# Kernel tuning notes

Hardware: AMD Instinct MI355X
Metric: run time of the kernel (lower is better)

## Reference

```python
import jax, jax.numpy as jnp
import numpy as np

D_MODEL = 256
NUM_HEADS = 8
DIM_HEAD = D_MODEL // NUM_HEADS
EPS = 1e-6
MASK_BIAS = -1.0e9


def setup_inputs() -> dict:
    key = jax.random.key(0)
    ks = jax.random.split(key, 10)
    B, S = 2, 4096
    x = jax.random.normal(ks[0], (B, S, D_MODEL), dtype=jnp.float32)
    pad_mask = jnp.zeros((B, S), dtype=jnp.float32)  # 1.0 => padded position
    scale = 1.0 / np.sqrt(D_MODEL)
    Wq = jax.random.normal(ks[1], (D_MODEL, D_MODEL), dtype=jnp.float32) * scale
    bq = jnp.zeros((D_MODEL,), dtype=jnp.float32)
    Wk = jax.random.normal(ks[2], (D_MODEL, D_MODEL), dtype=jnp.float32) * scale
    bk = jnp.zeros((D_MODEL,), dtype=jnp.float32)
    Wv = jax.random.normal(ks[3], (D_MODEL, D_MODEL), dtype=jnp.float32) * scale
    bv = jnp.zeros((D_MODEL,), dtype=jnp.float32)
    gamma = jnp.ones((D_MODEL,), dtype=jnp.float32)
    beta = jnp.zeros((D_MODEL,), dtype=jnp.float32)
    return {"x": x, "pad_mask": pad_mask, "Wq": Wq, "bq": bq, "Wk": Wk,
            "bk": bk, "Wv": Wv, "bv": bv, "gamma": gamma, "beta": beta}


def _layer_norm(h, gamma, beta):
    mu = jnp.mean(h, axis=-1, keepdims=True)
    var = jnp.mean(jnp.square(h - mu), axis=-1, keepdims=True)
    return gamma * (h - mu) * jax.lax.rsqrt(var + EPS) + beta


def reference(x, pad_mask, Wq, bq, Wk, bk, Wv, bv, gamma, beta):
    B, S, D = x.shape
    q = x @ Wq + bq  # [B,S,D]
    k = x @ Wk + bk
    v = x @ Wv + bv
    # split heads: [B,S,D] -> [B,H,S,Dh]
    def split(t):
        return t.reshape(B, S, NUM_HEADS, DIM_HEAD).transpose(0, 2, 1, 3)
    qh, kh, vh = split(q), split(k), split(v)
    w = jnp.einsum("bhqd,bhkd->bhqk", qh, kh)  # [B,H,S,S]
    # faithful to source: mask added BEFORE the 1/sqrt(dim_head) scaling
    w = w + pad_mask[:, None, None, :] * MASK_BIAS
    w = w / jnp.sqrt(jnp.float32(DIM_HEAD))
    attn = jax.nn.softmax(w, axis=-1)
    # dropout is identity at inference
    out = jnp.einsum("bhqk,bhkd->bhqd", attn, vh)  # [B,H,S,Dh]
    out = out.transpose(0, 2, 1, 3).reshape(B, S, D)
    return _layer_norm(out + x, gamma, beta)
```

## Files before the change

### kernel.cpp

```cpp
#include <hip/hip_runtime.h>
#include <hip/hip_bf16.h>

#define D_MODEL 256
#define NUM_HEADS 8
#define DIM_HEAD 32
#define SEQ 4096
#define BATCH 2
#define NROWS (BATCH * SEQ)
#define LN_EPS 1e-6f
#define MASK_BIAS -1.0e9f
#define SCALE 0.17677669529663687f
#define LOG2E 1.4426950408889634f

typedef __attribute__((ext_vector_type(8))) short short8;
typedef __attribute__((ext_vector_type(4))) float f32x4;

static __device__ __forceinline__ unsigned short f2b(float f) {
    union { __hip_bfloat16 b; unsigned short u; } cv;
    cv.b = __float2bfloat16(f);
    return cv.u;
}
static __device__ __forceinline__ unsigned int pk_bf16(float lo, float hi) {
    union { __hip_bfloat162 v; unsigned int u; } cv;
    cv.v = __float22bfloat162_rn(make_float2(lo, hi));
    return cv.u;
}
static __device__ __forceinline__ float exp2_raw(float x) {
#if __has_builtin(__builtin_amdgcn_exp2f)
    return __builtin_amdgcn_exp2f(x);
#else
    float r;
    asm volatile("v_exp_f32 %0, %1" : "=v"(r) : "v"(x));
    return r;
#endif
}
static __device__ __forceinline__ void load_lds16(const void* g, void* l) {
    __builtin_amdgcn_global_load_lds(
        (const __attribute__((address_space(1))) unsigned int*)g,
        (__attribute__((address_space(3))) unsigned int*)l, 16, 0, 0);
}

__global__ __launch_bounds__(256) void prep_kernel(
    const float* __restrict__ Wq, const float* __restrict__ Wk,
    const float* __restrict__ Wv,
    const float* __restrict__ bq, const float* __restrict__ bk,
    const float* __restrict__ bv,
    const float* __restrict__ pad,
    unsigned short* __restrict__ Wt, float* __restrict__ biasc,
    float* __restrict__ T2)
{
    const int blk = blockIdx.x;
    const int t = threadIdx.x;
    if (blk < 768) {
        const int w = blk >> 8;
        const int k = blk & 255;
        const float* W = (w == 0) ? Wq : (w == 1) ? Wk : Wv;
        Wt[(size_t)(w * 256 + t) * 256 + k] = f2b(W[(size_t)k * 256 + t]);
        if (k == 0) {
            const float* bb = (w == 0) ? bq : (w == 1) ? bk : bv;
            biasc[w * 256 + t] = bb[t];
        }
    } else {
        const int i = (blk - 768) * 256 + t;
        T2[i] = pad[i] * (MASK_BIAS * SCALE * LOG2E);
    }
}

__global__ __launch_bounds__(256) void qkv_mfma_kernel(
    const float* __restrict__ x, const unsigned short* __restrict__ Wt,
    const float* __restrict__ biasc,
    unsigned short* __restrict__ Qh, unsigned short* __restrict__ Kh,
    unsigned short* __restrict__ Vt)
{
    const int lane = threadIdx.x & 63;
    const int wid  = threadIdx.x >> 6;
    const int c    = lane & 15;
    const int quad = lane >> 4;

    const int r0 = (blockIdx.x >> 3) * 64 + wid * 16;
    const int n0 = (blockIdx.x & 7) * 96;

    f32x4 acc[6];
    float bias[6];
    #pragma unroll
    for (int t = 0; t < 6; t++) {
        acc[t] = (f32x4){0.f, 0.f, 0.f, 0.f};
        bias[t] = biasc[n0 + 16 * t + c];
    }

    const float* xp0 = x + (size_t)(r0 + c) * D_MODEL + quad * 8;
    const unsigned short* wp0 = Wt + (size_t)(n0 + c) * 256 + quad * 8;

    for (int k0 = 0; k0 < 256; k0 += 32) {
        const float4 a0 = *(const float4*)(xp0 + k0);
        const float4 a1 = *(const float4*)(xp0 + k0 + 4);
        union { unsigned int u[4]; short8 s; } af;
        af.u[0] = pk_bf16(a0.x, a0.y);
        af.u[1] = pk_bf16(a0.z, a0.w);
        af.u[2] = pk_bf16(a1.x, a1.y);
        af.u[3] = pk_bf16(a1.z, a1.w);
        #pragma unroll
        for (int t = 0; t < 6; t++) {
            const short8 bf = *(const short8*)(wp0 + (size_t)(16 * t) * 256 + k0);
            acc[t] = __builtin_amdgcn_mfma_f32_16x16x32_bf16(af.s, bf, acc[t], 0, 0, 0);
        }
    }

    #pragma unroll
    for (int t = 0; t < 6; t++) {
        const int col = n0 + 16 * t;
        const int mm  = col >> 8;
        const int dim = (col & 255) + c;
        const int h = dim >> 5, d = dim & 31;
        const int row = r0 + quad * 4;
        const int bb = row >> 12;
        const int s  = row & (SEQ - 1);
        const size_t bh = (size_t)(bb * NUM_HEADS + h);
        const float v0 = acc[t][0] + bias[t];
        const float v1 = acc[t][1] + bias[t];
        const float v2 = acc[t][2] + bias[t];
        const float v3 = acc[t][3] + bias[t];
        if (mm == 2) {
            uint2 pk = make_uint2(pk_bf16(v0, v1), pk_bf16(v2, v3));
            *(uint2*)(Vt + (bh * DIM_HEAD + d) * SEQ + s) = pk;
        } else {
            unsigned short* P = (mm == 0 ? Qh : Kh) + (bh * SEQ + s) * DIM_HEAD + d;
            P[0]  = f2b(v0);
            P[32] = f2b(v1);
            P[64] = f2b(v2);
            P[96] = f2b(v3);
        }
    }
}

__global__ __launch_bounds__(256, 4) void attn_mfma_kernel(
    const unsigned short* __restrict__ Qh, const unsigned short* __restrict__ Kh,
    const unsigned short* __restrict__ Vt, const float* __restrict__ T2,
    float* __restrict__ O)
{
    __shared__ __align__(16) unsigned short ldsK[2][64 * 32];
    __shared__ __align__(16) unsigned short ldsV[2][32 * 64];
    __shared__ __align__(16) float          ldsT[2][64];

    const int lane = threadIdx.x & 63;
    const int wid  = threadIdx.x >> 6;
    const int c    = lane & 15;
    const int quad = lane >> 4;

    const int gw = blockIdx.x;
    const int q0 = (gw & 63) * 64;
    const int h  = (gw >> 6) & (NUM_HEADS - 1);
    const int b  = gw >> 9;
    const size_t bh = (size_t)(b * NUM_HEADS + h);

    const float k2 = SCALE * LOG2E;
    const int perm = ((c & 12) << 1) | (c & 3);

    const unsigned short* Kb = Kh + bh * SEQ * DIM_HEAD;
    const unsigned short* Vb = Vt + bh * DIM_HEAD * SEQ;
    const float* Tb = T2 + (size_t)b * SEQ;

    const int qrow = q0 + wid * 16;
    const short8 qf = *(const short8*)(Qh + (bh * SEQ + qrow + c) * DIM_HEAD + quad * 8);

    union { unsigned int u[4]; short8 s; } ones;
    ones.u[0] = ones.u[1] = ones.u[2] = ones.u[3] = 0x3F803F80u;

    const int f0 = ((perm >> 1) ^ (perm >> 3)) & 3;
    const int f1 = (((perm + 4) >> 1) ^ ((perm + 4) >> 3)) & 3;
    const int kA = perm * 32 + ((quad ^ f0) << 3);
    const int kB = (perm + 4) * 32 + ((quad ^ f1) << 3);
    const int g0 = quad ^ (c & 7);
    const int vA0 = c * 64 + (g0 << 3);
    const int vA1 = c * 64 + ((g0 ^ 4) << 3);
    const int vB0 = (16 + c) * 64 + (g0 << 3);
    const int vB1 = (16 + c) * 64 + ((g0 ^ 4) << 3);

    const int skey = (lane >> 2);
    const int sgK  = lane & 3;
    const int sdim = lane >> 3;
    const int sgV  = lane & 7;

    f32x4 o0 = {0.f,0.f,0.f,0.f}, o1 = {0.f,0.f,0.f,0.f};
    f32x4 lacc = {0.f,0.f,0.f,0.f};
    const f32x4 z = {0.f, 0.f, 0.f, 0.f};

    auto stage = [&](int ch, int pb) {
        const int s0 = ch * 64;
        if (wid < 2) {
            #pragma unroll
            for (int jj = 0; jj < 2; jj++) {
                const int j = wid * 2 + jj;
                const int key = j * 16 + skey;
                const int f = ((key >> 1) ^ (key >> 3)) & 3;
                load_lds16(Kb + (size_t)(s0 + key) * 32 + ((sgK ^ f) << 3),
                           &ldsK[pb][j * 512]);
            }
        } else {
            #pragma unroll
            for (int jj = 0; jj < 2; jj++) {
                const int j = (wid - 2) * 2 + jj;
                const int dim = j * 8 + sdim;
                load_lds16(Vb + (size_t)dim * SEQ + s0 + ((sgV ^ (dim & 7)) << 3),
                           &ldsV[pb][j * 512]);
            }
            if (wid == 3 && lane < 16)
                load_lds16(Tb + s0 + lane * 4, &ldsT[pb][0]);
        }
    };

    auto sub = [&](int pb, int s) {
        const short8 kf0 = *(const short8*)&ldsK[pb][s * 1024 + kA];
        const short8 kf1 = *(const short8*)&ldsK[pb][s * 1024 + kB];
        const short8 vf0 = *(const short8*)&ldsV[pb][s ? vA1 : vA0];
        const short8 vf1 = *(const short8*)&ldsV[pb][s ? vB1 : vB0];
        const float4 t0 = *(const float4*)&ldsT[pb][s * 32 + quad * 8];
        const float4 t1 = *(const float4*)&ldsT[pb][s * 32 + quad * 8 + 4];

        const f32x4 st0 = __builtin_amdgcn_mfma_f32_16x16x32_bf16(kf0, qf, z, 0, 0, 0);
        const f32x4 st1 = __builtin_amdgcn_mfma_f32_16x16x32_bf16(kf1, qf, z, 0, 0, 0);

        float p[8];
        p[0] = exp2_raw(fmaf(st0[0], k2, t0.x));
        p[1] = exp2_raw(fmaf(st0[1], k2, t0.y));
        p[2] = exp2_raw(fmaf(st0[2], k2, t0.z));
        p[3] = exp2_raw(fmaf(st0[3], k2, t0.w));
        p[4] = exp2_raw(fmaf(st1[0], k2, t1.x));
        p[5] = exp2_raw(fmaf(st1[1], k2, t1.y));
        p[6] = exp2_raw(fmaf(st1[2], k2, t1.z));
        p[7] = exp2_raw(fmaf(st1[3], k2, t1.w));

        union { unsigned int u[4]; short8 s8; } pf;
        pf.u[0] = pk_bf16(p[0], p[1]);
        pf.u[1] = pk_bf16(p[2], p[3]);
        pf.u[2] = pk_bf16(p[4], p[5]);
        pf.u[3] = pk_bf16(p[6], p[7]);

        lacc = __builtin_amdgcn_mfma_f32_16x16x32_bf16(ones.s, pf.s8, lacc, 0, 0, 0);
        o0   = __builtin_amdgcn_mfma_f32_16x16x32_bf16(vf0,   pf.s8, o0,   0, 0, 0);
        o1   = __builtin_amdgcn_mfma_f32_16x16x32_bf16(vf1,   pf.s8, o1,   0, 0, 0);
    };

    stage(0, 0);
    __syncthreads();
    for (int ch = 0; ch < SEQ / 64; ++ch) {
        const int pb = ch & 1;
        stage((ch + 1) & 63, pb ^ 1);
        sub(pb, 0);
        sub(pb, 1);
        __syncthreads();
    }

    const float inv = 1.0f / lacc[0];
    float* op = O + ((size_t)(b * SEQ) + qrow + c) * D_MODEL + h * DIM_HEAD + quad * 4;
    *(float4*)op        = make_float4(o0[0]*inv, o0[1]*inv, o0[2]*inv, o0[3]*inv);
    *(float4*)(op + 16) = make_float4(o1[0]*inv, o1[1]*inv, o1[2]*inv, o1[3]*inv);
}

__global__ __launch_bounds__(256) void ln_kernel(
    float* AO,
    const float* __restrict__ x,
    const float* __restrict__ gamma, const float* __restrict__ beta)
{
    const int lane = threadIdx.x & 63;
    const int wid  = threadIdx.x >> 6;
    const size_t row = (size_t)blockIdx.x * 4 + wid;

    const float4 a  = ((const float4*)(AO + row * D_MODEL))[lane];
    const float4 xv = ((const float4*)(x + row * D_MODEL))[lane];
    float hv[4];
    hv[0] = a.x + xv.x;
    hv[1] = a.y + xv.y;
    hv[2] = a.z + xv.z;
    hv[3] = a.w + xv.w;

    float s = hv[0] + hv[1] + hv[2] + hv[3];
    #pragma unroll
    for (int off = 32; off > 0; off >>= 1) s += __shfl_xor(s, off, 64);
    const float mu = s * (1.0f / D_MODEL);

    float d0 = hv[0]-mu, d1 = hv[1]-mu, d2 = hv[2]-mu, d3 = hv[3]-mu;
    float ss = d0*d0 + d1*d1 + d2*d2 + d3*d3;
    #pragma unroll
    for (int off = 32; off > 0; off >>= 1) ss += __shfl_xor(ss, off, 64);
    const float rs = rsqrtf(ss * (1.0f / D_MODEL) + LN_EPS);

    const float4 g  = ((const float4*)gamma)[lane];
    const float4 bb = ((const float4*)beta)[lane];
    float4 y;
    y.x = g.x * d0 * rs + bb.x;
    y.y = g.y * d1 * rs + bb.y;
    y.z = g.z * d2 * rs + bb.z;
    y.w = g.w * d3 * rs + bb.w;
    ((float4*)(AO + row * D_MODEL))[lane] = y;
}

extern "C" void kernel_launch(void* const* d_in, const int* in_sizes, int n_in,
                              void* d_out, int out_size, void* d_ws, size_t ws_size,
                              hipStream_t stream)
{
    const float* x     = (const float*)d_in[0];
    const float* pad   = (const float*)d_in[1];
    const float* Wq    = (const float*)d_in[2];
    const float* bq    = (const float*)d_in[3];
    const float* Wk    = (const float*)d_in[4];
    const float* bk    = (const float*)d_in[5];
    const float* Wv    = (const float*)d_in[6];
    const float* bv    = (const float*)d_in[7];
    const float* gamma = (const float*)d_in[8];
    const float* beta  = (const float*)d_in[9];

    const size_t elems = (size_t)NROWS * D_MODEL;
    unsigned short* Qh = (unsigned short*)d_ws;
    unsigned short* Kh = Qh + elems;
    unsigned short* Vt = Kh + elems;
    float* T2 = (float*)(Vt + elems);
    unsigned short* Wt = (unsigned short*)(T2 + NROWS);
    float* biasc = (float*)(Wt + 768 * 256);
    float* AO = (float*)d_out;

    prep_kernel<<<800, 256, 0, stream>>>(Wq, Wk, Wv, bq, bk, bv, pad,
                                         Wt, biasc, T2);
    qkv_mfma_kernel<<<(NROWS / 64) * 8, 256, 0, stream>>>(x, Wt, biasc,
                                                          Qh, Kh, Vt);
    attn_mfma_kernel<<<BATCH * NUM_HEADS * (SEQ / 64), 256, 0, stream>>>(
        Qh, Kh, Vt, T2, AO);
    ln_kernel<<<NROWS / 4, 256, 0, stream>>>(AO, x, gamma, beta);
}
```

Measured before the change: 190.1 us.

## Triple-buffer K/V staging with explicit waitcnt and fold score scale into Q

The attention loop moves from double to triple buffering of K/V/mask tiles in LDS. It prefetches two chunks ahead and synchronises with manual s_waitcnt vmcnt plus a raw s_barrier, replacing __syncthreads. Separately, the softmax scale times log2e is folded into Q in the projection kernel, and the mask term is fed as the MFMA accumulator init, removing the per-element FMA before exp2. Risks are higher LDS use, which may reduce occupancy, fragile hand-counted vmcnt values, and a small precision change from rounding Q to bf16 after scaling.

```diff
diff --git a/kernel.cpp b/kernel.cpp
--- a/kernel.cpp
+++ b/kernel.cpp
@@ -11,6 +11,7 @@
 #define MASK_BIAS -1.0e9f
 #define SCALE 0.17677669529663687f
 #define LOG2E 1.4426950408889634f
+#define QSCALE (SCALE * LOG2E)
 
 typedef __attribute__((ext_vector_type(8))) short short8;
 typedef __attribute__((ext_vector_type(4))) float f32x4;
@@ -116,14 +117,17 @@
         const int bb = row >> 12;
         const int s  = row & (SEQ - 1);
         const size_t bh = (size_t)(bb * NUM_HEADS + h);
-        const float v0 = acc[t][0] + bias[t];
-        const float v1 = acc[t][1] + bias[t];
-        const float v2 = acc[t][2] + bias[t];
-        const float v3 = acc[t][3] + bias[t];
+        float v0 = acc[t][0] + bias[t];
+        float v1 = acc[t][1] + bias[t];
+        float v2 = acc[t][2] + bias[t];
+        float v3 = acc[t][3] + bias[t];
         if (mm == 2) {
             uint2 pk = make_uint2(pk_bf16(v0, v1), pk_bf16(v2, v3));
             *(uint2*)(Vt + (bh * DIM_HEAD + d) * SEQ + s) = pk;
         } else {
+            if (mm == 0) {
+                v0 *= QSCALE; v1 *= QSCALE; v2 *= QSCALE; v3 *= QSCALE;
+            }
             unsigned short* P = (mm == 0 ? Qh : Kh) + (bh * SEQ + s) * DIM_HEAD + d;
             P[0]  = f2b(v0);
             P[32] = f2b(v1);
@@ -138,9 +142,9 @@
     const unsigned short* __restrict__ Vt, const float* __restrict__ T2,
     float* __restrict__ O)
 {
-    __shared__ __align__(16) unsigned short ldsK[2][64 * 32];
-    __shared__ __align__(16) unsigned short ldsV[2][32 * 64];
-    __shared__ __align__(16) float          ldsT[2][64];
+    __shared__ __align__(16) unsigned short ldsK[3][64 * 32];
+    __shared__ __align__(16) unsigned short ldsV[3][32 * 64];
+    __shared__ __align__(16) float          ldsT[3][64];
 
     const int lane = threadIdx.x & 63;
     const int wid  = threadIdx.x >> 6;
@@ -153,7 +157,6 @@
     const int b  = gw >> 9;
     const size_t bh = (size_t)(b * NUM_HEADS + h);
 
-    const float k2 = SCALE * LOG2E;
     const int perm = ((c & 12) << 1) | (c & 3);
 
     const unsigned short* Kb = Kh + bh * SEQ * DIM_HEAD;
@@ -183,7 +186,6 @@
 
     f32x4 o0 = {0.f,0.f,0.f,0.f}, o1 = {0.f,0.f,0.f,0.f};
     f32x4 lacc = {0.f,0.f,0.f,0.f};
-    const f32x4 z = {0.f, 0.f, 0.f, 0.f};
 
     auto stage = [&](int ch, int pb) {
         const int s0 = ch * 64;
@@ -217,18 +219,20 @@
         const float4 t0 = *(const float4*)&ldsT[pb][s * 32 + quad * 8];
         const float4 t1 = *(const float4*)&ldsT[pb][s * 32 + quad * 8 + 4];
 
-        const f32x4 st0 = __builtin_amdgcn_mfma_f32_16x16x32_bf16(kf0, qf, z, 0, 0, 0);
-        const f32x4 st1 = __builtin_amdgcn_mfma_f32_16x16x32_bf16(kf1, qf, z, 0, 0, 0);
+        const f32x4 c0 = {t0.x, t0.y, t0.z, t0.w};
+        const f32x4 c1 = {t1.x, t1.y, t1.z, t1.w};
+        const f32x4 st0 = __builtin_amdgcn_mfma_f32_16x16x32_bf16(kf0, qf, c0, 0, 0, 0);
+        const f32x4 st1 = __builtin_amdgcn_mfma_f32_16x16x32_bf16(kf1, qf, c1, 0, 0, 0);
 
         float p[8];
-        p[0] = exp2_raw(fmaf(st0[0], k2, t0.x));
-        p[1] = exp2_raw(fmaf(st0[1], k2, t0.y));
-        p[2] = exp2_raw(fmaf(st0[2], k2, t0.z));
-        p[3] = exp2_raw(fmaf(st0[3], k2, t0.w));
-        p[4] = exp2_raw(fmaf(st1[0], k2, t1.x));
-        p[5] = exp2_raw(fmaf(st1[1], k2, t1.y));
-        p[6] = exp2_raw(fmaf(st1[2], k2, t1.z));
-        p[7] = exp2_raw(fmaf(st1[3], k2, t1.w));
+        p[0] = exp2_raw(st0[0]);
+        p[1] = exp2_raw(st0[1]);
+        p[2] = exp2_raw(st0[2]);
+        p[3] = exp2_raw(st0[3]);
+        p[4] = exp2_raw(st1[0]);
+        p[5] = exp2_raw(st1[1]);
+        p[6] = exp2_raw(st1[2]);
+        p[7] = exp2_raw(st1[3]);
 
         union { unsigned int u[4]; short8 s8; } pf;
         pf.u[0] = pk_bf16(p[0], p[1]);
@@ -242,13 +246,22 @@
     };
 
     stage(0, 0);
-    __syncthreads();
+    stage(1, 1);
+
+    int rb = 0;
+    int sb = 2;
     for (int ch = 0; ch < SEQ / 64; ++ch) {
-        const int pb = ch & 1;
-        stage((ch + 1) & 63, pb ^ 1);
-        sub(pb, 0);
-        sub(pb, 1);
-        __syncthreads();
+        if (wid == 3)
+            asm volatile("s_waitcnt vmcnt(3) lgkmcnt(0)" ::: "memory");
+        else
+            asm volatile("s_waitcnt vmcnt(2) lgkmcnt(0)" ::: "memory");
+        __builtin_amdgcn_s_barrier();
+        __builtin_amdgcn_sched_barrier(0);
+        stage((ch + 2) & 63, sb);
+        sub(rb, 0);
+        sub(rb, 1);
+        rb = (rb == 2) ? 0 : rb + 1;
+        sb = (sb == 2) ? 0 : sb + 1;
     }
 
     const float inv = 1.0f / lacc[0];
```

New measurement: 178.5 us. 1.07x faster.
